# Performance work log

Hardware: AMD Instinct MI355X
Metric: run time of the kernel (lower is better)

The kernel has to match this reference:

```python
import jax, jax.numpy as jnp
import numpy as np

B, T, C = 4, 1024, 1024
H = 16
DH = C // H  # 64


def setup_inputs() -> dict:
    key = jax.random.key(0)
    ks = jax.random.split(key, 10)
    s = 0.02
    return {
        "x": jax.random.normal(ks[0], (B, T, C), dtype=jnp.float32),
        "Wq": jax.random.normal(ks[1], (C, C), dtype=jnp.float32) * s,
        "bq": jnp.zeros((C,), dtype=jnp.float32),
        "Wk": jax.random.normal(ks[2], (C, C), dtype=jnp.float32) * s,
        "bk": jnp.zeros((C,), dtype=jnp.float32),
        "Wv": jax.random.normal(ks[3], (C, C), dtype=jnp.float32) * s,
        "bv": jnp.zeros((C,), dtype=jnp.float32),
        "Wp": jax.random.normal(ks[4], (C, C), dtype=jnp.float32) * s,
        "bp": jnp.zeros((C,), dtype=jnp.float32),
    }


def reference(x, Wq, bq, Wk, bk, Wv, bv, Wp, bp):
    b, t, c = x.shape
    # QKV projections, split into heads: [b, H, t, DH]
    def heads(y):
        return y.reshape(b, t, H, DH).transpose(0, 2, 1, 3)
    q = heads(x @ Wq + bq)
    k = heads(x @ Wk + bk)
    v = heads(x @ Wv + bv)
    # Causal attention. Original masks with -inf BEFORE scaling; -inf*scale is
    # still -inf, so mask-then-scale == scale-then-mask.
    scores = jnp.einsum("bhqd,bhkd->bhqk", q, k) * (DH ** -0.5)
    causal = jnp.tril(jnp.ones((t, t), dtype=bool))
    scores = jnp.where(causal, scores, -jnp.inf)
    attn = jax.nn.softmax(scores, axis=-1)  # dropout p=0.0 -> identity
    ctx = jnp.einsum("bhqk,bhkd->bhqd", attn, v)
    ctx = ctx.transpose(0, 2, 1, 3).reshape(b, t, c)
    return ctx @ Wp + bp
```

## Files before the change

### kernel.cpp

```cpp
#include <hip/hip_runtime.h>


typedef unsigned short ushort_t;
typedef __attribute__((ext_vector_type(8))) __bf16 bf16x8;
typedef __attribute__((ext_vector_type(8))) unsigned short us8;
typedef __attribute__((ext_vector_type(4))) unsigned short us4;
typedef __attribute__((ext_vector_type(4))) float f32x4;

#define AS1 __attribute__((address_space(1)))
#define AS3 __attribute__((address_space(3)))

__device__ __forceinline__ ushort_t f2bf(float f) {
  unsigned int u = __float_as_uint(f);
  u += 0x7fffu + ((u >> 16) & 1u);
  return (ushort_t)(u >> 16);
}


__global__ void cvt_x_kernel(const float* __restrict__ x, ushort_t* __restrict__ xb) {
  const int i = blockIdx.x * 256 + threadIdx.x;
  const float4 v = reinterpret_cast<const float4*>(x)[i];
  us4 o;
  o.x = f2bf(v.x); o.y = f2bf(v.y); o.z = f2bf(v.z); o.w = f2bf(v.w);
  reinterpret_cast<us4*>(xb)[i] = o;
}

__global__ void cvt_w4_kernel(const float* __restrict__ Wq, const float* __restrict__ Wk,
                              const float* __restrict__ Wv, const float* __restrict__ Wp,
                              ushort_t* __restrict__ WQKVT, ushort_t* __restrict__ WPT) {
  __shared__ float t[32][33];
  const int z = blockIdx.z;
  const float* W = (z == 0) ? Wq : (z == 1) ? Wk : (z == 2) ? Wv : Wp;
  ushort_t* Wt = (z == 3) ? WPT : (WQKVT + ((size_t)z << 20));
  const float wscale = (z == 0) ? 0.125f : 1.0f;
  const int n0 = blockIdx.x * 32, k0 = blockIdx.y * 32;
  const int tx = threadIdx.x, ty = threadIdx.y;
#pragma unroll
  for (int i = ty; i < 32; i += 8)
    t[i][tx] = W[(size_t)(k0 + i) * 1024 + n0 + tx];
  __syncthreads();
#pragma unroll
  for (int i = ty; i < 32; i += 8)
    Wt[(size_t)(n0 + i) * 1024 + k0 + tx] = f2bf(t[tx][i] * wscale);
}


__global__ __launch_bounds__(512) void gemm_qkv256_kernel(
    const ushort_t* __restrict__ A, const ushort_t* __restrict__ Bt,
    const float* __restrict__ bq, const float* __restrict__ bk,
    const float* __restrict__ bv, ushort_t* __restrict__ QKVB,
    ushort_t* __restrict__ VT) {
  __shared__ ushort_t smem[2][2][256 * 64];
  const int tid = threadIdx.x;
  const int wave = tid >> 6, lane = tid & 63;
  const int lgrp = lane >> 4, lmod = lane & 15;
  const int wr = wave >> 2, wc = wave & 3;
  const int swz = (blockIdx.x & 7) * 24 + (blockIdx.x >> 3);
  const int row0 = (swz / 12) * 256, col0 = (swz % 12) * 256;

  const ushort_t* Ag = A + (size_t)row0 * 1024;
  const ushort_t* Bg = Bt + (size_t)col0 * 1024;

  const int srow = lane >> 3;
  const int sslot = (lane & 7) ^ srow;
  const int xm = lmod & 7;

  auto stage_half = [&](int buf, int t, int h) {
#pragma unroll
    for (int op = 0; op < 2; ++op) {
      const ushort_t* G = (op ? Bg : Ag) + t * 64;
#pragma unroll
      for (int i = 0; i < 2; ++i) {
        const int c0 = h * 1024 + i * 512 + wave * 64;
        __builtin_amdgcn_global_load_lds(
            (AS1 void*)(G + (size_t)((c0 >> 3) + srow) * 1024 + sslot * 8),
            (AS3 void*)((char*)&smem[buf][op][0] + c0 * 16), 16, 0, 0);
      }
    }
  };

  f32x4 acc[8][4] = {};
  constexpr int nt = 16;

  stage_half(0, 0, 0);
  stage_half(0, 0, 1);

  for (int t = 0; t < nt; ++t) {
    const int cur = t & 1, nxt = cur ^ 1;
    const char* cA = (const char*)&smem[cur][0][0];
    const char* cB = (const char*)&smem[cur][1][0];

    if (t + 1 < nt) {
      stage_half(nxt, t + 1, 0);
      asm volatile("s_waitcnt vmcnt(4)" ::: "memory");
    } else {
      asm volatile("s_waitcnt vmcnt(0)" ::: "memory");
    }
    __builtin_amdgcn_sched_barrier(0);
    __builtin_amdgcn_s_barrier();

    bf16x8 a0[8], b0[4], a1[8], b1[4];
#pragma unroll
    for (int ni = 0; ni < 4; ++ni)
      b0[ni] = *reinterpret_cast<const bf16x8*>(
          cB + (wc * 64 + ni * 16 + lmod) * 128 + ((lgrp ^ xm) << 4));
#pragma unroll
    for (int mi = 0; mi < 8; ++mi)
      a0[mi] = *reinterpret_cast<const bf16x8*>(
          cA + (wr * 128 + mi * 16 + lmod) * 128 + ((lgrp ^ xm) << 4));

    __builtin_amdgcn_s_setprio(1);
#pragma unroll
    for (int mi = 0; mi < 4; ++mi)
#pragma unroll
      for (int ni = 0; ni < 4; ++ni)
        acc[mi][ni] = __builtin_amdgcn_mfma_f32_16x16x32_bf16(a0[mi], b0[ni], acc[mi][ni], 0, 0, 0);
    __builtin_amdgcn_s_setprio(0);

#pragma unroll
    for (int ni = 0; ni < 4; ++ni)
      b1[ni] = *reinterpret_cast<const bf16x8*>(
          cB + (wc * 64 + ni * 16 + lmod) * 128 + (((4 | lgrp) ^ xm) << 4));
#pragma unroll
    for (int mi = 0; mi < 8; ++mi)
      a1[mi] = *reinterpret_cast<const bf16x8*>(
          cA + (wr * 128 + mi * 16 + lmod) * 128 + (((4 | lgrp) ^ xm) << 4));

    __builtin_amdgcn_s_setprio(1);
#pragma unroll
    for (int mi = 0; mi < 4; ++mi)
#pragma unroll
      for (int ni = 0; ni < 4; ++ni)
        acc[4 + mi][ni] = __builtin_amdgcn_mfma_f32_16x16x32_bf16(a0[4 + mi], b0[ni], acc[4 + mi][ni], 0, 0, 0);
    __builtin_amdgcn_s_setprio(0);

    if (t + 1 < nt) stage_half(nxt, t + 1, 1);

    __builtin_amdgcn_s_setprio(1);
#pragma unroll
    for (int mi = 0; mi < 8; ++mi)
#pragma unroll
      for (int ni = 0; ni < 4; ++ni)
        acc[mi][ni] = __builtin_amdgcn_mfma_f32_16x16x32_bf16(a1[mi], b1[ni], acc[mi][ni], 0, 0, 0);
    __builtin_amdgcn_s_setprio(0);

    __builtin_amdgcn_s_barrier();
  }

  if (col0 < 2048) {
    const float* bsel = (col0 < 1024) ? bq : bk;
    const float bsc = (col0 < 1024) ? 0.125f : 1.0f;
    float bvv[4];
#pragma unroll
    for (int ni = 0; ni < 4; ++ni)
      bvv[ni] = bsel[(col0 & 1023) + wc * 64 + ni * 16 + lmod] * bsc;
#pragma unroll
    for (int mi = 0; mi < 8; ++mi) {
#pragma unroll
      for (int ni = 0; ni < 4; ++ni) {
        const int col = col0 + wc * 64 + ni * 16 + lmod;
#pragma unroll
        for (int r = 0; r < 4; ++r) {
          const int row = row0 + wr * 128 + mi * 16 + lgrp * 4 + r;
          QKVB[(size_t)row * 3072 + col] = f2bf(acc[mi][ni][r] + bvv[ni]);
        }
      }
    }
  } else {
    float bvv[4];
#pragma unroll
    for (int ni = 0; ni < 4; ++ni)
      bvv[ni] = bv[(col0 - 2048) + wc * 64 + ni * 16 + lmod];
#pragma unroll
    for (int mi = 0; mi < 8; ++mi) {
#pragma unroll
      for (int ni = 0; ni < 4; ++ni) {
        const int hd = (col0 - 2048) + wc * 64 + ni * 16 + lmod;
        const int R = row0 + wr * 128 + mi * 16 + lgrp * 4;
        const int bb = R >> 10, tl = R & 1023;
        us4 o;
#pragma unroll
        for (int r = 0; r < 4; ++r) o[r] = f2bf(acc[mi][ni][r] + bvv[ni]);
        *reinterpret_cast<us4*>(VT + ((size_t)(bb * 16 + (hd >> 6)) * 64 + (hd & 63)) * 1024 + tl) = o;
      }
    }
  }
}


__global__ __launch_bounds__(256, 2) void gemm_proj_kernel(
    const ushort_t* __restrict__ A, const ushort_t* __restrict__ Bt,
    const float* __restrict__ bias, float* __restrict__ Cout) {
  constexpr int BM = 64, WR = 32, MFR = 2, NIT = 3;
  __shared__ ushort_t As[BM * 32];
  __shared__ ushort_t Bs[128 * 32];
  const int tid = threadIdx.x;
  const int wave = tid >> 6, lane = tid & 63;
  const int lgrp = lane >> 4, lmod = lane & 15;
  const int wr = wave >> 1, wc = wave & 1;
  const int cpx = gridDim.x >> 3;
  const int swz = (blockIdx.x & 7) * cpx + (blockIdx.x >> 3);
  const int row0 = (swz / 8) * BM, col0 = (swz % 8) * 128;

  f32x4 acc[MFR][4] = {};

  for (int k0 = 0; k0 < 1024; k0 += 32) {
#pragma unroll
    for (int it = 0; it < NIT; ++it) {
      const int c0 = it * 256 + wave * 64;
      const int c = c0 + lane;
      if (c0 < BM * 4) {
        const int r = c >> 2, kk = (c & 3) << 3;
        __builtin_amdgcn_global_load_lds(
            (AS1 void*)(A + (size_t)(row0 + r) * 1024 + k0 + kk),
            (AS3 void*)(As + (c0 << 3)), 16, 0, 0);
      } else {
        const int cb = c - BM * 4;
        const int r = cb >> 2, kk = (cb & 3) << 3;
        __builtin_amdgcn_global_load_lds(
            (AS1 void*)(Bt + (size_t)(col0 + r) * 1024 + k0 + kk),
            (AS3 void*)(Bs + ((c0 - BM * 4) << 3)), 16, 0, 0);
      }
    }
    __syncthreads();

    bf16x8 af[MFR], bfr[4];
#pragma unroll
    for (int i = 0; i < MFR; ++i)
      af[i] = *reinterpret_cast<const bf16x8*>(&As[(wr * WR + i * 16 + lmod) * 32 + lgrp * 8]);
#pragma unroll
    for (int i = 0; i < 4; ++i)
      bfr[i] = *reinterpret_cast<const bf16x8*>(&Bs[(wc * 64 + i * 16 + lmod) * 32 + lgrp * 8]);
    __builtin_amdgcn_s_setprio(1);
#pragma unroll
    for (int mi = 0; mi < MFR; ++mi)
#pragma unroll
      for (int ni = 0; ni < 4; ++ni)
        acc[mi][ni] = __builtin_amdgcn_mfma_f32_16x16x32_bf16(af[mi], bfr[ni], acc[mi][ni], 0, 0, 0);
    __builtin_amdgcn_s_setprio(0);
    __syncthreads();
  }

  float bvv[4];
#pragma unroll
  for (int ni = 0; ni < 4; ++ni) bvv[ni] = bias[col0 + wc * 64 + ni * 16 + lmod];
#pragma unroll
  for (int mi = 0; mi < MFR; ++mi)
#pragma unroll
    for (int ni = 0; ni < 4; ++ni) {
      const int col = col0 + wc * 64 + ni * 16 + lmod;
#pragma unroll
      for (int r = 0; r < 4; ++r) {
        const int row = row0 + wr * WR + mi * 16 + lgrp * 4 + r;
        Cout[(size_t)row * 1024 + col] = acc[mi][ni][r] + bvv[ni];
      }
    }
}


__global__ __launch_bounds__(256, 2) void attn_kernel(
    const ushort_t* __restrict__ QKV, const ushort_t* __restrict__ VT,
    ushort_t* __restrict__ Og) {
  const int bid = blockIdx.x;
  const int swz = (bid & 7) * 64 + (bid >> 3);
  const int p = swz & 7, bh = swz >> 3;
  const int b = bh >> 4, h = bh & 15;
  const int jmax = 15 - p;
  const int tid = threadIdx.x;
  const int wave = tid >> 6, lane = tid & 63;
  const int lgrp = lane >> 4, lmod = lane & 15;

  __shared__ ushort_t Ks[64 * 72];
  __shared__ ushort_t Vs[64 * 72];
  __shared__ ushort_t Ps[4][16 * 72];

  const size_t xrow0 = (size_t)b * 1024;
  const int qlo = p * 64 + wave * 16;
  const int qhi = jmax * 64 + wave * 16;

  bf16x8 qfl[2], qfh[2];
#pragma unroll
  for (int ks = 0; ks < 2; ++ks) {
    qfl[ks] = *reinterpret_cast<const bf16x8*>(
        QKV + (xrow0 + qlo + lmod) * 3072 + h * 64 + ks * 32 + lgrp * 8);
    qfh[ks] = *reinterpret_cast<const bf16x8*>(
        QKV + (xrow0 + qhi + lmod) * 3072 + h * 64 + ks * 32 + lgrp * 8);
  }

  f32x4 ol[4] = {}, oh[4] = {};
  float ll[4] = {0.f, 0.f, 0.f, 0.f}, lh[4] = {0.f, 0.f, 0.f, 0.f};

  const int sr = tid >> 3;
  const int scc = (tid & 7) << 3;
  us8 kreg0, kreg1, vreg0, vreg1;

  auto load_tile = [&](int j) {
    const ushort_t* kp = QKV + (xrow0 + j * 64 + sr) * 3072 + 1024 + h * 64 + scc;
    kreg0 = *reinterpret_cast<const us8*>(kp);
    kreg1 = *reinterpret_cast<const us8*>(kp + 32 * 3072);
    const ushort_t* vp = VT + ((size_t)bh * 64 + sr) * 1024 + j * 64 + scc;
    vreg0 = *reinterpret_cast<const us8*>(vp);
    vreg1 = *reinterpret_cast<const us8*>(vp + 32 * 1024);
  };
  auto write_tile = [&]() {
    *reinterpret_cast<us8*>(&Ks[sr * 72 + scc]) = kreg0;
    *reinterpret_cast<us8*>(&Ks[(32 + sr) * 72 + scc]) = kreg1;
    *reinterpret_cast<us8*>(&Vs[sr * 72 + scc]) = vreg0;
    *reinterpret_cast<us8*>(&Vs[(32 + sr) * 72 + scc]) = vreg1;
  };

  auto step = [&](const bf16x8* qf, f32x4* oacc, float* lsum, bool diag) {
    f32x4 s[4];
    __builtin_amdgcn_s_setprio(1);
#pragma unroll
    for (int cg = 0; cg < 4; ++cg) {
      f32x4 a = {};
#pragma unroll
      for (int ks = 0; ks < 2; ++ks) {
        bf16x8 kf = *reinterpret_cast<const bf16x8*>(
            &Ks[(cg * 16 + lmod) * 72 + ks * 32 + lgrp * 8]);
        a = __builtin_amdgcn_mfma_f32_16x16x32_bf16(qf[ks], kf, a, 0, 0, 0);
      }
      s[cg] = a;
    }
    __builtin_amdgcn_s_setprio(0);
    if (diag) {
      const int qloc = wave * 16 + lgrp * 4;
#pragma unroll
      for (int cg = 0; cg < 4; ++cg) {
        const int kcol = cg * 16 + lmod;
#pragma unroll
        for (int r = 0; r < 4; ++r)
          if (kcol > qloc + r) s[cg][r] = -1e30f;
      }
    }
#pragma unroll
    for (int cg = 0; cg < 4; ++cg)
#pragma unroll
      for (int r = 0; r < 4; ++r) s[cg][r] = __expf(s[cg][r]);
#pragma unroll
    for (int r = 0; r < 4; ++r)
      lsum[r] += (s[0][r] + s[1][r]) + (s[2][r] + s[3][r]);
#pragma unroll
    for (int cg = 0; cg < 4; ++cg)
#pragma unroll
      for (int r = 0; r < 4; ++r)
        Ps[wave][(lgrp * 4 + r) * 72 + cg * 16 + lmod] = f2bf(s[cg][r]);
    __builtin_amdgcn_s_setprio(1);
#pragma unroll
    for (int ks = 0; ks < 2; ++ks) {
      bf16x8 pf = *reinterpret_cast<const bf16x8*>(
          &Ps[wave][lmod * 72 + ks * 32 + lgrp * 8]);
#pragma unroll
      for (int dhg = 0; dhg < 4; ++dhg) {
        bf16x8 vf = *reinterpret_cast<const bf16x8*>(
            &Vs[(dhg * 16 + lmod) * 72 + ks * 32 + lgrp * 8]);
        oacc[dhg] = __builtin_amdgcn_mfma_f32_16x16x32_bf16(pf, vf, oacc[dhg], 0, 0, 0);
      }
    }
    __builtin_amdgcn_s_setprio(0);
  };

  load_tile(0);
  for (int j = 0; j <= jmax; ++j) {
    __syncthreads();
    write_tile();
    __syncthreads();
    if (j < jmax) load_tile(j + 1);
    if (j <= p) step(qfl, ol, ll, j == p);
    step(qfh, oh, lh, j == jmax);
  }

#pragma unroll
  for (int m = 1; m <= 8; m <<= 1)
#pragma unroll
    for (int r = 0; r < 4; ++r) {
      ll[r] += __shfl_xor(ll[r], m);
      lh[r] += __shfl_xor(lh[r], m);
    }

#pragma unroll
  for (int dhg = 0; dhg < 4; ++dhg) {
    const int col = h * 64 + dhg * 16 + lmod;
#pragma unroll
    for (int r = 0; r < 4; ++r) {
      Og[(xrow0 + qlo + lgrp * 4 + r) * 1024 + col] = f2bf(ol[dhg][r] / ll[r]);
      Og[(xrow0 + qhi + lgrp * 4 + r) * 1024 + col] = f2bf(oh[dhg][r] / lh[r]);
    }
  }
}


extern "C" void kernel_launch(void* const* d_in, const int* in_sizes, int n_in,
                              void* d_out, int out_size, void* d_ws, size_t ws_size,
                              hipStream_t stream) {
  const float* x  = (const float*)d_in[0];
  const float* Wq = (const float*)d_in[1];
  const float* bq = (const float*)d_in[2];
  const float* Wk = (const float*)d_in[3];
  const float* bk = (const float*)d_in[4];
  const float* Wv = (const float*)d_in[5];
  const float* bv = (const float*)d_in[6];
  const float* Wp = (const float*)d_in[7];
  const float* bp = (const float*)d_in[8];
  float* out = (float*)d_out;

  char* ws = (char*)d_ws;
  ushort_t* XB    = (ushort_t*)(ws);
  ushort_t* WQKVT = (ushort_t*)(ws + ( 8ull << 20));
  ushort_t* WPT   = (ushort_t*)(ws + (14ull << 20));
  ushort_t* QKVB  = (ushort_t*)(ws + (16ull << 20));
  ushort_t* VT    = (ushort_t*)(ws + (40ull << 20));

  cvt_x_kernel<<<4096, 256, 0, stream>>>(x, XB);
  cvt_w4_kernel<<<dim3(32, 32, 4), dim3(32, 8), 0, stream>>>(Wq, Wk, Wv, Wp, WQKVT, WPT);
  gemm_qkv256_kernel<<<192, 512, 0, stream>>>(XB, WQKVT, bq, bk, bv, QKVB, VT);
  attn_kernel<<<512, 256, 0, stream>>>(QKVB, VT, XB);
  gemm_proj_kernel<<<512, 256, 0, stream>>>(XB, WPT, bp, out);
}
```

Before: 93.84 us.

## Restructure QKV GEMM main loop into four-phase ping-pong with quarter-tile prefetch

```diff
diff --git a/kernel.cpp b/kernel.cpp
--- a/kernel.cpp
+++ b/kernel.cpp
@@ -14,6 +14,12 @@
   unsigned int u = __float_as_uint(f);
   u += 0x7fffu + ((u >> 16) & 1u);
   return (ushort_t)(u >> 16);
+}
+
+__device__ __forceinline__ ushort_t f2bf_hw(float f) {
+  union { __bf16 b; ushort_t u; } cv;
+  cv.b = (__bf16)f;
+  return cv.u;
 }
 
 
@@ -43,6 +49,10 @@
   for (int i = ty; i < 32; i += 8)
     Wt[(size_t)(n0 + i) * 1024 + k0 + tx] = f2bf(t[tx][i] * wscale);
 }
+
+#define BAR_PIN() do { __builtin_amdgcn_sched_barrier(0); \
+                       __builtin_amdgcn_s_barrier();      \
+                       __builtin_amdgcn_sched_barrier(0); } while (0)
 
 
 __global__ __launch_bounds__(512) void gemm_qkv256_kernel(
@@ -65,86 +75,107 @@
   const int sslot = (lane & 7) ^ srow;
   const int xm = lmod & 7;
 
-  auto stage_half = [&](int buf, int t, int h) {
-#pragma unroll
-    for (int op = 0; op < 2; ++op) {
-      const ushort_t* G = (op ? Bg : Ag) + t * 64;
-#pragma unroll
-      for (int i = 0; i < 2; ++i) {
-        const int c0 = h * 1024 + i * 512 + wave * 64;
-        __builtin_amdgcn_global_load_lds(
-            (AS1 void*)(G + (size_t)((c0 >> 3) + srow) * 1024 + sslot * 8),
-            (AS3 void*)((char*)&smem[buf][op][0] + c0 * 16), 16, 0, 0);
-      }
+  auto stage_q = [&](int buf, int t, int q) {
+    const int op = q >> 1, rh = q & 1;
+    const ushort_t* G = (op ? Bg : Ag) + t * 64;
+#pragma unroll
+    for (int i = 0; i < 2; ++i) {
+      const int c0 = rh * 1024 + i * 512 + wave * 64;
+      __builtin_amdgcn_global_load_lds(
+          (AS1 void*)(G + (size_t)((c0 >> 3) + srow) * 1024 + sslot * 8),
+          (AS3 void*)((char*)&smem[buf][op][0] + c0 * 16), 16, 0, 0);
     }
   };
 
   f32x4 acc[8][4] = {};
   constexpr int nt = 16;
 
-  stage_half(0, 0, 0);
-  stage_half(0, 0, 1);
+  stage_q(0, 0, 0); stage_q(0, 0, 1); stage_q(0, 0, 2); stage_q(0, 0, 3);
+  asm volatile("s_waitcnt vmcnt(0)" ::: "memory");
+  BAR_PIN();
+
+  bf16x8 a[4][2], b[4][2];
+  auto ldf = [&](const char* base, int row, int slot) {
+    return *reinterpret_cast<const bf16x8*>(base + row * 128 + (slot << 4));
+  };
 
   for (int t = 0; t < nt; ++t) {
     const int cur = t & 1, nxt = cur ^ 1;
     const char* cA = (const char*)&smem[cur][0][0];
     const char* cB = (const char*)&smem[cur][1][0];
-
-    if (t + 1 < nt) {
-      stage_half(nxt, t + 1, 0);
-      asm volatile("s_waitcnt vmcnt(4)" ::: "memory");
-    } else {
-      asm volatile("s_waitcnt vmcnt(0)" ::: "memory");
-    }
-    __builtin_amdgcn_sched_barrier(0);
-    __builtin_amdgcn_s_barrier();
-
-    bf16x8 a0[8], b0[4], a1[8], b1[4];
-#pragma unroll
-    for (int ni = 0; ni < 4; ++ni)
-      b0[ni] = *reinterpret_cast<const bf16x8*>(
-          cB + (wc * 64 + ni * 16 + lmod) * 128 + ((lgrp ^ xm) << 4));
-#pragma unroll
-    for (int mi = 0; mi < 8; ++mi)
-      a0[mi] = *reinterpret_cast<const bf16x8*>(
-          cA + (wr * 128 + mi * 16 + lmod) * 128 + ((lgrp ^ xm) << 4));
-
+    const bool pre = (t + 1 < nt);
+    const int s0 = lgrp ^ xm, s1 = (4 + lgrp) ^ xm;
+
+#pragma unroll
+    for (int ni = 0; ni < 2; ++ni) {
+      b[ni][0] = ldf(cB, wc * 64 + ni * 16 + lmod, s0);
+      b[ni][1] = ldf(cB, wc * 64 + ni * 16 + lmod, s1);
+    }
+#pragma unroll
+    for (int mi = 0; mi < 4; ++mi) {
+      a[mi][0] = ldf(cA, wr * 128 + mi * 16 + lmod, s0);
+      a[mi][1] = ldf(cA, wr * 128 + mi * 16 + lmod, s1);
+    }
+    if (pre) { stage_q(nxt, t + 1, 0); stage_q(nxt, t + 1, 1); }
+    BAR_PIN();
     __builtin_amdgcn_s_setprio(1);
 #pragma unroll
     for (int mi = 0; mi < 4; ++mi)
 #pragma unroll
-      for (int ni = 0; ni < 4; ++ni)
-        acc[mi][ni] = __builtin_amdgcn_mfma_f32_16x16x32_bf16(a0[mi], b0[ni], acc[mi][ni], 0, 0, 0);
-    __builtin_amdgcn_s_setprio(0);
-
-#pragma unroll
-    for (int ni = 0; ni < 4; ++ni)
-      b1[ni] = *reinterpret_cast<const bf16x8*>(
-          cB + (wc * 64 + ni * 16 + lmod) * 128 + (((4 | lgrp) ^ xm) << 4));
-#pragma unroll
-    for (int mi = 0; mi < 8; ++mi)
-      a1[mi] = *reinterpret_cast<const bf16x8*>(
-          cA + (wr * 128 + mi * 16 + lmod) * 128 + (((4 | lgrp) ^ xm) << 4));
-
+      for (int ni = 0; ni < 2; ++ni) {
+        acc[mi][ni] = __builtin_amdgcn_mfma_f32_16x16x32_bf16(a[mi][0], b[ni][0], acc[mi][ni], 0, 0, 0);
+        acc[mi][ni] = __builtin_amdgcn_mfma_f32_16x16x32_bf16(a[mi][1], b[ni][1], acc[mi][ni], 0, 0, 0);
+      }
+    __builtin_amdgcn_s_setprio(0);
+    BAR_PIN();
+
+#pragma unroll
+    for (int ni = 2; ni < 4; ++ni) {
+      b[ni][0] = ldf(cB, wc * 64 + ni * 16 + lmod, s0);
+      b[ni][1] = ldf(cB, wc * 64 + ni * 16 + lmod, s1);
+    }
+    if (pre) stage_q(nxt, t + 1, 2);
+    BAR_PIN();
     __builtin_amdgcn_s_setprio(1);
 #pragma unroll
     for (int mi = 0; mi < 4; ++mi)
 #pragma unroll
-      for (int ni = 0; ni < 4; ++ni)
-        acc[4 + mi][ni] = __builtin_amdgcn_mfma_f32_16x16x32_bf16(a0[4 + mi], b0[ni], acc[4 + mi][ni], 0, 0, 0);
-    __builtin_amdgcn_s_setprio(0);
-
-    if (t + 1 < nt) stage_half(nxt, t + 1, 1);
-
-    __builtin_amdgcn_s_setprio(1);
-#pragma unroll
-    for (int mi = 0; mi < 8; ++mi)
-#pragma unroll
-      for (int ni = 0; ni < 4; ++ni)
-        acc[mi][ni] = __builtin_amdgcn_mfma_f32_16x16x32_bf16(a1[mi], b1[ni], acc[mi][ni], 0, 0, 0);
-    __builtin_amdgcn_s_setprio(0);
-
-    __builtin_amdgcn_s_barrier();
+      for (int ni = 2; ni < 4; ++ni) {
+        acc[mi][ni] = __builtin_amdgcn_mfma_f32_16x16x32_bf16(a[mi][0], b[ni][0], acc[mi][ni], 0, 0, 0);
+        acc[mi][ni] = __builtin_amdgcn_mfma_f32_16x16x32_bf16(a[mi][1], b[ni][1], acc[mi][ni], 0, 0, 0);
+      }
+    __builtin_amdgcn_s_setprio(0);
+    BAR_PIN();
+
+#pragma unroll
+    for (int mi = 0; mi < 4; ++mi) {
+      a[mi][0] = ldf(cA, wr * 128 + (4 + mi) * 16 + lmod, s0);
+      a[mi][1] = ldf(cA, wr * 128 + (4 + mi) * 16 + lmod, s1);
+    }
+    if (pre) stage_q(nxt, t + 1, 3);
+    BAR_PIN();
+    __builtin_amdgcn_s_setprio(1);
+#pragma unroll
+    for (int mi = 0; mi < 4; ++mi)
+#pragma unroll
+      for (int ni = 0; ni < 2; ++ni) {
+        acc[4 + mi][ni] = __builtin_amdgcn_mfma_f32_16x16x32_bf16(a[mi][0], b[ni][0], acc[4 + mi][ni], 0, 0, 0);
+        acc[4 + mi][ni] = __builtin_amdgcn_mfma_f32_16x16x32_bf16(a[mi][1], b[ni][1], acc[4 + mi][ni], 0, 0, 0);
+      }
+    __builtin_amdgcn_s_setprio(0);
+    BAR_PIN();
+
+    __builtin_amdgcn_s_setprio(1);
+#pragma unroll
+    for (int mi = 0; mi < 4; ++mi)
+#pragma unroll
+      for (int ni = 2; ni < 4; ++ni) {
+        acc[4 + mi][ni] = __builtin_amdgcn_mfma_f32_16x16x32_bf16(a[mi][0], b[ni][0], acc[4 + mi][ni], 0, 0, 0);
+        acc[4 + mi][ni] = __builtin_amdgcn_mfma_f32_16x16x32_bf16(a[mi][1], b[ni][1], acc[4 + mi][ni], 0, 0, 0);
+      }
+    __builtin_amdgcn_s_setprio(0);
+    if (pre) asm volatile("s_waitcnt vmcnt(0)" ::: "memory");
+    BAR_PIN();
   }
 
   if (col0 < 2048) {
@@ -345,7 +376,7 @@
     for (int cg = 0; cg < 4; ++cg)
 #pragma unroll
       for (int r = 0; r < 4; ++r)
-        Ps[wave][(lgrp * 4 + r) * 72 + cg * 16 + lmod] = f2bf(s[cg][r]);
+        Ps[wave][(lgrp * 4 + r) * 72 + cg * 16 + lmod] = f2bf_hw(s[cg][r]);
     __builtin_amdgcn_s_setprio(1);
 #pragma unroll
     for (int ks = 0; ks < 2; ++ks) {
@@ -384,8 +415,8 @@
     const int col = h * 64 + dhg * 16 + lmod;
 #pragma unroll
     for (int r = 0; r < 4; ++r) {
-      Og[(xrow0 + qlo + lgrp * 4 + r) * 1024 + col] = f2bf(ol[dhg][r] / ll[r]);
-      Og[(xrow0 + qhi + lgrp * 4 + r) * 1024 + col] = f2bf(oh[dhg][r] / lh[r]);
+      Og[(xrow0 + qlo + lgrp * 4 + r) * 1024 + col] = f2bf_hw(ol[dhg][r] / ll[r]);
+      Og[(xrow0 + qhi + lgrp * 4 + r) * 1024 + col] = f2bf_hw(oh[dhg][r] / lh[r]);
     }
   }
 }
```

Measured after the change: 95.29 us. About the same (+1.5%).
